# Performance work log

Hardware: AMD Instinct MI355X
Metric: run time of the kernel (lower is better)

## Reference

```python
import jax, jax.numpy as jnp
import numpy as np

HIDDEN = 128
HEADS = 8
HEAD_DIM = HIDDEN // HEADS  # 16
N_NODE_TYPES = 3
N_EDGE_TYPES = 5
N_SRC = 50000
N_DST = 50000
N_EDGES = 800000
SCALE = float(np.sqrt(HEAD_DIM))


def setup_inputs() -> dict:
    key = jax.random.key(0)
    ks = jax.random.split(key, 12)
    lim = 1.0 / np.sqrt(HIDDEN)  # torch Linear default init range
    # xavier_uniform for [H, d, d] relation tensors: gain*sqrt(6/(fan_in+fan_out))
    xav = float(np.sqrt(6.0 / (HEAD_DIM + HEAD_DIM)))
    return {
        "x_src": jax.random.normal(ks[0], (N_SRC, HIDDEN), jnp.float32),
        "x_dst": jax.random.normal(ks[1], (N_DST, HIDDEN), jnp.float32),
        "edge_index": jax.random.randint(ks[2], (2, N_EDGES), 0, N_DST),
        "src_type": 0,
        "edge_type": 1,
        "dst_type": 2,
        "k_w": jax.random.uniform(ks[3], (N_NODE_TYPES, HIDDEN, HIDDEN), jnp.float32, -lim, lim),
        "k_b": jax.random.uniform(ks[4], (N_NODE_TYPES, HIDDEN), jnp.float32, -lim, lim),
        "q_w": jax.random.uniform(ks[5], (N_NODE_TYPES, HIDDEN, HIDDEN), jnp.float32, -lim, lim),
        "q_b": jax.random.uniform(ks[6], (N_NODE_TYPES, HIDDEN), jnp.float32, -lim, lim),
        "v_w": jax.random.uniform(ks[7], (N_NODE_TYPES, HIDDEN, HIDDEN), jnp.float32, -lim, lim),
        "v_b": jax.random.uniform(ks[8], (N_NODE_TYPES, HIDDEN), jnp.float32, -lim, lim),
        "relation_att": jax.random.uniform(ks[9], (N_EDGE_TYPES, HEADS, HEAD_DIM, HEAD_DIM), jnp.float32, -xav, xav),
        "relation_msg": jax.random.uniform(ks[10], (N_EDGE_TYPES, HEADS, HEAD_DIM, HEAD_DIM), jnp.float32, -xav, xav),
        "relation_pri": jnp.ones((N_EDGE_TYPES, HEADS), jnp.float32),
    }


def reference(x_src, x_dst, edge_index, src_type, edge_type, dst_type,
              k_w, k_b, q_w, q_b, v_w, v_b,
              relation_att, relation_msg, relation_pri):
    n_dst = x_dst.shape[0]
    # relation-specific node projections (torch Linear: x @ W.T + b)
    k = (x_src @ k_w[src_type].T + k_b[src_type]).reshape(-1, HEADS, HEAD_DIM)
    v = (x_src @ v_w[src_type].T + v_b[src_type]).reshape(-1, HEADS, HEAD_DIM)
    q = (x_dst @ q_w[dst_type].T + q_b[dst_type]).reshape(-1, HEADS, HEAD_DIM)

    src_idx, dst_idx = edge_index[0], edge_index[1]
    # gather + per-edge relation matmul: [E, H, d]
    k_edge = jnp.einsum('ehi,hio->eho', k[src_idx], relation_att[edge_type])
    att = (k_edge * q[dst_idx]).sum(-1) / SCALE + relation_pri[edge_type][None, :]  # [E, H]

    # segmented softmax over incoming edges per dst node.
    # torch scatter_reduce amax starts from a zero-initialized buffer -> max(0, seg_max)
    seg_max = jnp.maximum(jax.ops.segment_max(att, dst_idx, num_segments=n_dst), 0.0)
    att_exp = jnp.exp(att - seg_max[dst_idx])
    seg_sum = jnp.maximum(jax.ops.segment_sum(att_exp, dst_idx, num_segments=n_dst), 1e-8)
    att_n = att_exp / seg_sum[dst_idx]  # [E, H]

    # messages + weighted scatter-add aggregation
    msg = jnp.einsum('ehi,hio->eho', v[src_idx], relation_msg[edge_type])  # [E, H, d]
    out = jax.ops.segment_sum(att_n[..., None] * msg, dst_idx, num_segments=n_dst)
    return out.reshape(n_dst, HIDDEN)
```

## Files before the change

### kernel.cpp

```cpp
#include <hip/hip_runtime.h>

#define HIDDEN 128
#define HEADS 8
#define HDIM 16
#define BW 64

typedef unsigned int uint;
typedef unsigned short ushort;
typedef __attribute__((ext_vector_type(8))) short bfrag;
typedef __attribute__((ext_vector_type(4))) float f32x4;

__device__ inline ushort f2bf(float f) {
    uint u = __float_as_uint(f);
    uint r = ((u >> 16) & 1u) + 0x7fffu;
    return (ushort)((u + r) >> 16);
}
__device__ inline float bf2f(ushort h) { return __uint_as_float((uint)h << 16); }
__device__ inline float bfl(uint u) { return __uint_as_float(u << 16); }
__device__ inline float bfh(uint u) { return __uint_as_float(u & 0xffff0000u); }

__device__ inline int frag_addr(int k, int n) {
    int ks = k >> 5, kr = k & 31, nt = n >> 4;
    int lane = ((kr >> 3) << 4) | (n & 15);
    return ((ks * 8 + nt) * 64 + lane) * 8 + (kr & 7);
}

__global__ void k1a_weights_zero(
    const float* __restrict__ k_w, const float* __restrict__ k_b,
    const float* __restrict__ q_w, const float* __restrict__ q_b,
    const float* __restrict__ v_w, const float* __restrict__ v_b,
    const float* __restrict__ r_att, const float* __restrict__ r_msg,
    const int* __restrict__ stp, const int* __restrict__ etp, const int* __restrict__ dtp,
    ushort* __restrict__ WkHi, ushort* __restrict__ WvHi, ushort* __restrict__ WqHi,
    float* __restrict__ bk, float* __restrict__ bv, float* __restrict__ bq,
    int* __restrict__ deg, int n_dst)
{
    int idx = blockIdx.x * 256 + threadIdx.x;
    for (int i = idx; i < n_dst; i += 64 * 256) deg[i] = 0;

    int st = stp[0], et = etp[0], dt = dtp[0];
    int c = idx >> 7, j = idx & 127;
    int h = j >> 4, o = j & 15;
    const float* kw = k_w + (size_t)st * HIDDEN * HIDDEN;
    const float* vw = v_w + (size_t)st * HIDDEN * HIDDEN;
    const float* ra = r_att + (size_t)et * HEADS * HDIM * HDIM + h * HDIM * HDIM + o;
    const float* rm = r_msg + (size_t)et * HEADS * HDIM * HDIM + h * HDIM * HDIM + o;
    float sk = 0.f, sv = 0.f;
#pragma unroll
    for (int i = 0; i < HDIM; ++i) {
        sk += kw[(h * HDIM + i) * HIDDEN + c] * ra[i * HDIM];
        sv += vw[(h * HDIM + i) * HIDDEN + c] * rm[i * HDIM];
    }
    float sq = q_w[(size_t)dt * HIDDEN * HIDDEN + (size_t)j * HIDDEN + c];
    int fa = frag_addr(c, j);
    WkHi[fa] = f2bf(sk);
    WvHi[fa] = f2bf(sv);
    WqHi[fa] = f2bf(sq);
    if (idx < HIDDEN) {
        float sb = 0.f, sbv = 0.f;
#pragma unroll
        for (int i = 0; i < HDIM; ++i) {
            sb  += k_b[st * HIDDEN + h * HDIM + i] * ra[i * HDIM];
            sbv += v_b[st * HIDDEN + h * HDIM + i] * rm[i * HDIM];
        }
        bk[idx] = sb;
        bv[idx] = sbv;
        bq[idx] = q_b[dt * HIDDEN + idx];
    }
}

__global__ __launch_bounds__(256, 5) void k1b_proj_countfill(
    const float* __restrict__ x_src, const float* __restrict__ x_dst,
    const ushort* __restrict__ WkHi, const ushort* __restrict__ WvHi,
    const ushort* __restrict__ WqHi,
    const float* __restrict__ bk, const float* __restrict__ bv,
    const float* __restrict__ bq,
    ushort* __restrict__ kr16, ushort* __restrict__ vm16,
    float* __restrict__ qout, int n_src, int n_dst, int nsb, int nprojb,
    const int* __restrict__ ei, int* __restrict__ deg,
    ushort* __restrict__ bucket, int n_edges, int nfb)
{
    __shared__ float xs[32 * 132];
    int blk = blockIdx.x;

    if ((blk % 5) == 4) {
        int fidx = blk / 5;
        if (fidx >= nfb) return;
        int t = fidx * 256 + threadIdx.x;
        int base = t * 4;
        if (base >= n_edges) return;
        if (base + 3 < n_edges) {
            int4 ss = *(const int4*)(ei + base);
            int4 dd = *(const int4*)(ei + n_edges + base);
            int r0 = atomicAdd(&deg[dd.x], 1); if (r0 < BW) bucket[(size_t)dd.x * BW + r0] = (ushort)ss.x;
            int r1 = atomicAdd(&deg[dd.y], 1); if (r1 < BW) bucket[(size_t)dd.y * BW + r1] = (ushort)ss.y;
            int r2 = atomicAdd(&deg[dd.z], 1); if (r2 < BW) bucket[(size_t)dd.z * BW + r2] = (ushort)ss.z;
            int r3 = atomicAdd(&deg[dd.w], 1); if (r3 < BW) bucket[(size_t)dd.w * BW + r3] = (ushort)ss.w;
        } else {
            for (int e = base; e < n_edges; ++e) {
                int d = ei[n_edges + e];
                int r = atomicAdd(&deg[d], 1);
                if (r < BW) bucket[(size_t)d * BW + r] = (ushort)ei[e];
            }
        }
        return;
    }

    int pidx = blk - blk / 5;
    if (pidx >= nprojb) return;
    int is_src = (pidx < nsb) ? 1 : 0;
    int brow0 = (is_src ? pidx : pidx - nsb) * 32;
    int n = is_src ? n_src : n_dst;
    const float* x = is_src ? x_src : x_dst;
    int t = threadIdx.x;

    {
        const float4* xg = (const float4*)x;
#pragma unroll
        for (int k = 0; k < 4; ++k) {
            int fi = t + k * 256;
            int r = fi >> 5, c4 = fi & 31;
            int row = brow0 + r;
            float4 v = xg[(size_t)(row < n ? row : n - 1) * 32 + c4];
            *(float4*)&xs[r * 132 + c4 * 4] = v;
        }
    }
    __syncthreads();

    int w = t >> 6, l = t & 63;
    int l15 = l & 15, kgrp = l >> 4;
    int nthalf = w & 1;
    int rtile = w >> 1;
    int rowbase = brow0 + rtile * 16;

    bfrag ahi[4], alo[4];
#pragma unroll
    for (int ks = 0; ks < 4; ++ks) {
        const float* xr = &xs[(rtile * 16 + l15) * 132 + ks * 32 + kgrp * 8];
        float4 x0 = *(const float4*)xr;
        float4 x1 = *(const float4*)(xr + 4);
        float xv[8] = {x0.x, x0.y, x0.z, x0.w, x1.x, x1.y, x1.z, x1.w};
#pragma unroll
        for (int b = 0; b < 8; ++b) {
            ushort hb = f2bf(xv[b]);
            ahi[ks][b] = (short)hb;
            alo[ks][b] = (short)f2bf(xv[b] - bf2f(hb));
        }
    }

    if (is_src) {
        const bfrag* Fk = (const bfrag*)WkHi;
        const bfrag* Fv = (const bfrag*)WvHi;
#pragma unroll
        for (int nt4 = 0; nt4 < 4; ++nt4) {
            int nt = nthalf * 4 + nt4;
            f32x4 ak = (f32x4){0.f, 0.f, 0.f, 0.f};
            f32x4 av = (f32x4){0.f, 0.f, 0.f, 0.f};
#pragma unroll
            for (int ks = 0; ks < 4; ++ks) {
                int fi = (ks * 8 + nt) * 64 + l;
                bfrag wk = Fk[fi], wv = Fv[fi];
                ak = __builtin_amdgcn_mfma_f32_16x16x32_bf16(ahi[ks], wk, ak, 0, 0, 0);
                ak = __builtin_amdgcn_mfma_f32_16x16x32_bf16(alo[ks], wk, ak, 0, 0, 0);
                av = __builtin_amdgcn_mfma_f32_16x16x32_bf16(ahi[ks], wv, av, 0, 0, 0);
                av = __builtin_amdgcn_mfma_f32_16x16x32_bf16(alo[ks], wv, av, 0, 0, 0);
            }
            int col = nt * 16 + l15;
            float bkc = bk[col], bvc = bv[col];
#pragma unroll
            for (int r = 0; r < 4; ++r) {
                int row = rowbase + kgrp * 4 + r;
                if (row < n) {
                    kr16[(size_t)row * HIDDEN + col] = f2bf(ak[r] + bkc);
                    vm16[(size_t)row * HIDDEN + col] = f2bf(av[r] + bvc);
                }
            }
        }
    } else {
        const bfrag* Fq = (const bfrag*)WqHi;
#pragma unroll
        for (int nt4 = 0; nt4 < 4; ++nt4) {
            int nt = nthalf * 4 + nt4;
            f32x4 aq = (f32x4){0.f, 0.f, 0.f, 0.f};
#pragma unroll
            for (int ks = 0; ks < 4; ++ks) {
                int fi = (ks * 8 + nt) * 64 + l;
                bfrag wq = Fq[fi];
                aq = __builtin_amdgcn_mfma_f32_16x16x32_bf16(ahi[ks], wq, aq, 0, 0, 0);
                aq = __builtin_amdgcn_mfma_f32_16x16x32_bf16(alo[ks], wq, aq, 0, 0, 0);
            }
            int col = nt * 16 + l15;
            float bqc = bq[col];
#pragma unroll
            for (int r = 0; r < 4; ++r) {
                int row = rowbase + kgrp * 4 + r;
                if (row < n) qout[(size_t)row * HIDDEN + col] = aq[r] + bqc;
            }
        }
    }
}

__global__ void fused_gather_kernel(const ushort* __restrict__ kr16,
                                    const ushort* __restrict__ vm16,
                                    const float* __restrict__ q,
                                    const float* __restrict__ pri,
                                    const int* __restrict__ etp,
                                    const int* __restrict__ deg,
                                    const ushort* __restrict__ bucket,
                                    float* __restrict__ out, int n_dst)
{
    int wave = (int)((blockIdx.x * 256 + threadIdx.x) >> 6);
    int l = threadIdx.x & 63;
    if (wave >= n_dst) return;
    int d = wave;
    int h = l >> 3;
    int e = l & 7;
    int len = deg[d]; if (len > BW) len = BW;
    const ushort* buck = bucket + (size_t)d * BW;

    const float4* qp = (const float4*)(q + (size_t)d * HIDDEN + h * HDIM);
    float4 q0 = qp[0], q1 = qp[1], q2 = qp[2], q3 = qp[3];
    float prih = pri[etp[0] * HEADS + h];

    float m = 0.0f;
    float ssum = 0.0f;
    float accx = 0.0f, accy = 0.0f;

    for (int i0 = 0; i0 < len; i0 += 8) {
        int ie = i0 + e;
        bool valid = ie < len;
        int s = buck[valid ? ie : 0];

        const uint4* kp = (const uint4*)(kr16 + (size_t)s * HIDDEN + h * HDIM);
        uint4 ka = kp[0], kb = kp[1];
        float dot =
            bfl(ka.x) * q0.x + bfh(ka.x) * q0.y + bfl(ka.y) * q0.z + bfh(ka.y) * q0.w +
            bfl(ka.z) * q1.x + bfh(ka.z) * q1.y + bfl(ka.w) * q1.z + bfh(ka.w) * q1.w +
            bfl(kb.x) * q2.x + bfh(kb.x) * q2.y + bfl(kb.y) * q2.z + bfh(kb.y) * q2.w +
            bfl(kb.z) * q3.x + bfh(kb.z) * q3.y + bfl(kb.w) * q3.z + bfh(kb.w) * q3.w;
        float a = valid ? (dot * 0.25f + prih) : -3.0e38f;

        float pm = a;
        pm = fmaxf(pm, __shfl_xor(pm, 1));
        pm = fmaxf(pm, __shfl_xor(pm, 2));
        pm = fmaxf(pm, __shfl_xor(pm, 4));
        float mnew = fmaxf(m, pm);
        float c = __expf(m - mnew);
        float w = valid ? __expf(a - mnew) : 0.0f;
        float S = w;
        S += __shfl_xor(S, 1);
        S += __shfl_xor(S, 2);
        S += __shfl_xor(S, 4);
        ssum = ssum * c + S;
        accx *= c;
        accy *= c;
        m = mnew;

#pragma unroll
        for (int ee = 0; ee < 8; ++ee) {
            int se = __shfl(s, ee);
            float we = __shfl(w, (l & 56) | ee);
            uint vv = *(const uint*)(vm16 + (size_t)se * HIDDEN + 2 * l);
            accx += we * bfl(vv);
            accy += we * bfh(vv);
        }
    }

    float inv = 1.0f / fmaxf(ssum, 1e-8f);
    float2 o; o.x = accx * inv; o.y = accy * inv;
    *(float2*)(out + (size_t)d * HIDDEN + 2 * l) = o;
}

extern "C" void kernel_launch(void* const* d_in, const int* in_sizes, int n_in,
                              void* d_out, int out_size, void* d_ws, size_t ws_size,
                              hipStream_t stream)
{
    const float* x_src = (const float*)d_in[0];
    const float* x_dst = (const float*)d_in[1];
    const int*   ei    = (const int*)d_in[2];
    const int*   stp   = (const int*)d_in[3];
    const int*   etp   = (const int*)d_in[4];
    const int*   dtp   = (const int*)d_in[5];
    const float* k_w   = (const float*)d_in[6];
    const float* k_b   = (const float*)d_in[7];
    const float* q_w   = (const float*)d_in[8];
    const float* q_b   = (const float*)d_in[9];
    const float* v_w   = (const float*)d_in[10];
    const float* v_b   = (const float*)d_in[11];
    const float* r_att = (const float*)d_in[12];
    const float* r_msg = (const float*)d_in[13];
    const float* r_pri = (const float*)d_in[14];

    int n_src   = in_sizes[0] / HIDDEN;
    int n_dst   = in_sizes[1] / HIDDEN;
    int n_edges = in_sizes[2] / 2;
    float* out = (float*)d_out;

    char* p = (char*)d_ws;
    ushort* kr16 = (ushort*)p;            p += (size_t)n_src * HIDDEN * sizeof(ushort);
    ushort* vm16 = (ushort*)p;            p += (size_t)n_src * HIDDEN * sizeof(ushort);
    float*  qv   = (float*)p;             p += (size_t)n_dst * HIDDEN * sizeof(float);
    ushort* bucket = (ushort*)p;          p += (size_t)n_dst * BW * sizeof(ushort);
    int* deg     = (int*)p;               p += (size_t)n_dst * sizeof(int);
    float* bk = (float*)p;                p += HIDDEN * sizeof(float);
    float* bv = (float*)p;                p += HIDDEN * sizeof(float);
    float* bq = (float*)p;                p += HIDDEN * sizeof(float);
    ushort* WkHi = (ushort*)p;            p += HIDDEN * HIDDEN * sizeof(ushort);
    ushort* WvHi = (ushort*)p;            p += HIDDEN * HIDDEN * sizeof(ushort);
    ushort* WqHi = (ushort*)p;            p += HIDDEN * HIDDEN * sizeof(ushort);

    k1a_weights_zero<<<64, 256, 0, stream>>>(
        k_w, k_b, q_w, q_b, v_w, v_b, r_att, r_msg, stp, etp, dtp,
        WkHi, WvHi, WqHi, bk, bv, bq, deg, n_dst);

    int nsb = (n_src + 31) / 32;
    int ndb = (n_dst + 31) / 32;
    int nprojb = nsb + ndb;
    int nfb = (n_edges / 4 + 256) / 256;
    int grid1 = 5 * nfb;
    int grid2 = ((nprojb + 3) / 4) * 5;
    int grid = grid1 > grid2 ? grid1 : grid2;
    k1b_proj_countfill<<<grid, 256, 0, stream>>>(
        x_src, x_dst, WkHi, WvHi, WqHi, bk, bv, bq,
        kr16, vm16, qv, n_src, n_dst, nsb, nprojb,
        ei, deg, bucket, n_edges, nfb);

    fused_gather_kernel<<<(int)(((size_t)n_dst * 64 + 255) / 256), 256, 0, stream>>>(
        kr16, vm16, qv, r_pri, etp, deg, bucket, out, n_dst);
}
```

Baseline: 128.3 us.

## Preload weight fragments into registers and process 16 edges per gather iteration

In the projection kernel, all MFMA weight fragments are loaded into registers up front, before the activation conversion, so global-load latency overlaps with the bf16 split work. The occupancy hint drops from 5 to 4 blocks to make room for the extra registers. In the fused gather kernel, the online-softmax loop now handles two batches of 8 edges per iteration, which issues more independent K/V gathers per pass and halves the number of shuffle reductions. This raises register pressure and may reduce occupancy.

```diff
diff --git a/kernel.cpp b/kernel.cpp
--- a/kernel.cpp
+++ b/kernel.cpp
@@ -69,7 +69,7 @@
     }
 }
 
-__global__ __launch_bounds__(256, 5) void k1b_proj_countfill(
+__global__ __launch_bounds__(256, 4) void k1b_proj_countfill(
     const float* __restrict__ x_src, const float* __restrict__ x_dst,
     const ushort* __restrict__ WkHi, const ushort* __restrict__ WvHi,
     const ushort* __restrict__ WqHi,
@@ -133,6 +133,31 @@
     int rtile = w >> 1;
     int rowbase = brow0 + rtile * 16;
 
+    bfrag wk[4][4], wv[4][4];
+    if (is_src) {
+        const bfrag* Fk = (const bfrag*)WkHi;
+        const bfrag* Fv = (const bfrag*)WvHi;
+#pragma unroll
+        for (int nt4 = 0; nt4 < 4; ++nt4) {
+#pragma unroll
+            for (int ks = 0; ks < 4; ++ks) {
+                int fi = (ks * 8 + nthalf * 4 + nt4) * 64 + l;
+                wk[nt4][ks] = Fk[fi];
+                wv[nt4][ks] = Fv[fi];
+            }
+        }
+    } else {
+        const bfrag* Fq = (const bfrag*)WqHi;
+#pragma unroll
+        for (int nt4 = 0; nt4 < 4; ++nt4) {
+#pragma unroll
+            for (int ks = 0; ks < 4; ++ks) {
+                int fi = (ks * 8 + nthalf * 4 + nt4) * 64 + l;
+                wk[nt4][ks] = Fq[fi];
+            }
+        }
+    }
+
     bfrag ahi[4], alo[4];
 #pragma unroll
     for (int ks = 0; ks < 4; ++ks) {
@@ -149,23 +174,18 @@
     }
 
     if (is_src) {
-        const bfrag* Fk = (const bfrag*)WkHi;
-        const bfrag* Fv = (const bfrag*)WvHi;
 #pragma unroll
         for (int nt4 = 0; nt4 < 4; ++nt4) {
-            int nt = nthalf * 4 + nt4;
             f32x4 ak = (f32x4){0.f, 0.f, 0.f, 0.f};
             f32x4 av = (f32x4){0.f, 0.f, 0.f, 0.f};
 #pragma unroll
             for (int ks = 0; ks < 4; ++ks) {
-                int fi = (ks * 8 + nt) * 64 + l;
-                bfrag wk = Fk[fi], wv = Fv[fi];
-                ak = __builtin_amdgcn_mfma_f32_16x16x32_bf16(ahi[ks], wk, ak, 0, 0, 0);
-                ak = __builtin_amdgcn_mfma_f32_16x16x32_bf16(alo[ks], wk, ak, 0, 0, 0);
-                av = __builtin_amdgcn_mfma_f32_16x16x32_bf16(ahi[ks], wv, av, 0, 0, 0);
-                av = __builtin_amdgcn_mfma_f32_16x16x32_bf16(alo[ks], wv, av, 0, 0, 0);
-            }
-            int col = nt * 16 + l15;
+                ak = __builtin_amdgcn_mfma_f32_16x16x32_bf16(ahi[ks], wk[nt4][ks], ak, 0, 0, 0);
+                ak = __builtin_amdgcn_mfma_f32_16x16x32_bf16(alo[ks], wk[nt4][ks], ak, 0, 0, 0);
+                av = __builtin_amdgcn_mfma_f32_16x16x32_bf16(ahi[ks], wv[nt4][ks], av, 0, 0, 0);
+                av = __builtin_amdgcn_mfma_f32_16x16x32_bf16(alo[ks], wv[nt4][ks], av, 0, 0, 0);
+            }
+            int col = (nthalf * 4 + nt4) * 16 + l15;
             float bkc = bk[col], bvc = bv[col];
 #pragma unroll
             for (int r = 0; r < 4; ++r) {
@@ -177,19 +197,15 @@
             }
         }
     } else {
-        const bfrag* Fq = (const bfrag*)WqHi;
 #pragma unroll
         for (int nt4 = 0; nt4 < 4; ++nt4) {
-            int nt = nthalf * 4 + nt4;
             f32x4 aq = (f32x4){0.f, 0.f, 0.f, 0.f};
 #pragma unroll
             for (int ks = 0; ks < 4; ++ks) {
-                int fi = (ks * 8 + nt) * 64 + l;
-                bfrag wq = Fq[fi];
-                aq = __builtin_amdgcn_mfma_f32_16x16x32_bf16(ahi[ks], wq, aq, 0, 0, 0);
-                aq = __builtin_amdgcn_mfma_f32_16x16x32_bf16(alo[ks], wq, aq, 0, 0, 0);
-            }
-            int col = nt * 16 + l15;
+                aq = __builtin_amdgcn_mfma_f32_16x16x32_bf16(ahi[ks], wk[nt4][ks], aq, 0, 0, 0);
+                aq = __builtin_amdgcn_mfma_f32_16x16x32_bf16(alo[ks], wk[nt4][ks], aq, 0, 0, 0);
+            }
+            int col = (nthalf * 4 + nt4) * 16 + l15;
             float bqc = bq[col];
 #pragma unroll
             for (int r = 0; r < 4; ++r) {
@@ -226,28 +242,40 @@
     float ssum = 0.0f;
     float accx = 0.0f, accy = 0.0f;
 
-    for (int i0 = 0; i0 < len; i0 += 8) {
-        int ie = i0 + e;
-        bool valid = ie < len;
-        int s = buck[valid ? ie : 0];
-
-        const uint4* kp = (const uint4*)(kr16 + (size_t)s * HIDDEN + h * HDIM);
-        uint4 ka = kp[0], kb = kp[1];
-        float dot =
-            bfl(ka.x) * q0.x + bfh(ka.x) * q0.y + bfl(ka.y) * q0.z + bfh(ka.y) * q0.w +
-            bfl(ka.z) * q1.x + bfh(ka.z) * q1.y + bfl(ka.w) * q1.z + bfh(ka.w) * q1.w +
-            bfl(kb.x) * q2.x + bfh(kb.x) * q2.y + bfl(kb.y) * q2.z + bfh(kb.y) * q2.w +
-            bfl(kb.z) * q3.x + bfh(kb.z) * q3.y + bfl(kb.w) * q3.z + bfh(kb.w) * q3.w;
-        float a = valid ? (dot * 0.25f + prih) : -3.0e38f;
-
-        float pm = a;
+    for (int i0 = 0; i0 < len; i0 += 16) {
+        int ieA = i0 + e, ieB = i0 + 8 + e;
+        bool vA = ieA < len, vB = ieB < len;
+        int sA = buck[vA ? ieA : 0];
+        int sB = buck[vB ? ieB : 0];
+
+        const uint4* kpA = (const uint4*)(kr16 + (size_t)sA * HIDDEN + h * HDIM);
+        const uint4* kpB = (const uint4*)(kr16 + (size_t)sB * HIDDEN + h * HDIM);
+        uint4 kaA = kpA[0], kbA = kpA[1];
+        uint4 kaB = kpB[0], kbB = kpB[1];
+
+        float dotA =
+            bfl(kaA.x) * q0.x + bfh(kaA.x) * q0.y + bfl(kaA.y) * q0.z + bfh(kaA.y) * q0.w +
+            bfl(kaA.z) * q1.x + bfh(kaA.z) * q1.y + bfl(kaA.w) * q1.z + bfh(kaA.w) * q1.w +
+            bfl(kbA.x) * q2.x + bfh(kbA.x) * q2.y + bfl(kbA.y) * q2.z + bfh(kbA.y) * q2.w +
+            bfl(kbA.z) * q3.x + bfh(kbA.z) * q3.y + bfl(kbA.w) * q3.z + bfh(kbA.w) * q3.w;
+        float dotB =
+            bfl(kaB.x) * q0.x + bfh(kaB.x) * q0.y + bfl(kaB.y) * q0.z + bfh(kaB.y) * q0.w +
+            bfl(kaB.z) * q1.x + bfh(kaB.z) * q1.y + bfl(kaB.w) * q1.z + bfh(kaB.w) * q1.w +
+            bfl(kbB.x) * q2.x + bfh(kbB.x) * q2.y + bfl(kbB.y) * q2.z + bfh(kbB.y) * q2.w +
+            bfl(kbB.z) * q3.x + bfh(kbB.z) * q3.y + bfl(kbB.w) * q3.z + bfh(kbB.w) * q3.w;
+
+        float aA = vA ? (dotA * 0.25f + prih) : -3.0e38f;
+        float aB = vB ? (dotB * 0.25f + prih) : -3.0e38f;
+
+        float pm = fmaxf(aA, aB);
         pm = fmaxf(pm, __shfl_xor(pm, 1));
         pm = fmaxf(pm, __shfl_xor(pm, 2));
         pm = fmaxf(pm, __shfl_xor(pm, 4));
         float mnew = fmaxf(m, pm);
         float c = __expf(m - mnew);
-        float w = valid ? __expf(a - mnew) : 0.0f;
-        float S = w;
+        float wA = vA ? __expf(aA - mnew) : 0.0f;
+        float wB = vB ? __expf(aB - mnew) : 0.0f;
+        float S = wA + wB;
         S += __shfl_xor(S, 1);
         S += __shfl_xor(S, 2);
         S += __shfl_xor(S, 4);
@@ -258,11 +286,21 @@
 
 #pragma unroll
         for (int ee = 0; ee < 8; ++ee) {
-            int se = __shfl(s, ee);
-            float we = __shfl(w, (l & 56) | ee);
+            int se = __shfl(sA, ee);
+            float we = __shfl(wA, (l & 56) | ee);
             uint vv = *(const uint*)(vm16 + (size_t)se * HIDDEN + 2 * l);
             accx += we * bfl(vv);
             accy += we * bfh(vv);
+        }
+        if (i0 + 8 < len) {
+#pragma unroll
+            for (int ee = 0; ee < 8; ++ee) {
+                int se = __shfl(sB, ee);
+                float we = __shfl(wB, (l & 56) | ee);
+                uint vv = *(const uint*)(vm16 + (size_t)se * HIDDEN + 2 * l);
+                accx += we * bfl(vv);
+                accy += we * bfh(vv);
+            }
         }
     }
 
```

Result: slower. 167.2 us (+30.3%).
